# Kernel optimization log

Hardware: AMD Instinct MI355X
Metric: run time of the kernel (lower is better)

The kernel has to match this reference:

```python
import jax, jax.numpy as jnp
import numpy as np

B, T, E = 16, 4096, 768
NEG = -10000000000.0

def setup_inputs() -> dict:
    key = jax.random.key(0)
    k1, k2, k3, k4 = jax.random.split(key, 4)
    query = jax.random.normal(k1, (B, E), dtype=jnp.float32)
    context = jax.random.normal(k2, (B, T, E), dtype=jnp.float32)
    mask = jax.random.randint(k3, (B, T), 0, 2, dtype=jnp.int32)
    # guarantee at least one unmasked position per row
    mask = mask.at[:, 0].set(1)
    v_w = jax.random.normal(k4, (2 * E,), dtype=jnp.float32) * (1.0 / np.sqrt(2 * E))
    return {"query": query, "context": context, "mask": mask, "v_w": v_w}

def reference(query, context, mask, v_w):
    # query: [b,e] -> broadcast to [b,t,e]; cat with context -> [b,t,2e]
    q = jnp.broadcast_to(query[:, None, :], context.shape)
    # score = tanh(cat([q, c])) . v_w ; split dot to avoid materializing concat
    scores = jnp.tanh(q) @ v_w[:context.shape[-1]] + jnp.tanh(context) @ v_w[context.shape[-1]:]  # [b,t]
    scores = jnp.where(mask < 1, NEG, scores)
    attn = jax.nn.softmax(scores, axis=-1)              # [b,t]
    return jnp.einsum("bt,bte->be", attn, context)      # [b,e]
```

## Files before the change

### kernel.cpp

```cpp
#include <hip/hip_runtime.h>

constexpr int Bc = 16;
constexpr int Tc = 4096;
constexpr int Ec = 768;
constexpr int PSTRIDE = Ec + 2;

__device__ __forceinline__ float fast_tanh(float x) {
    x = fminf(15.0f, fmaxf(-15.0f, x));
    float e = __expf(2.0f * x);
    return (e - 1.0f) * __builtin_amdgcn_rcpf(e + 1.0f);
}

__device__ __forceinline__ float dot_tanh4(float4 c, float4 w) {
    float s;
    s = fast_tanh(c.x) * w.x;
    s = fmaf(fast_tanh(c.y), w.y, s);
    s = fmaf(fast_tanh(c.z), w.z, s);
    s = fmaf(fast_tanh(c.w), w.w, s);
    return s;
}

__device__ __forceinline__ float4 upd4(float4 o, float alpha, float p, float4 c) {
    return make_float4(fmaf(o.x, alpha, p * c.x),
                       fmaf(o.y, alpha, p * c.y),
                       fmaf(o.z, alpha, p * c.z),
                       fmaf(o.w, alpha, p * c.w));
}

template<int C>
__global__ __launch_bounds__(256) void attn_partial(
    const float* __restrict__ ctx, const int* __restrict__ mask,
    const float* __restrict__ v_w, float* __restrict__ ws)
{
    constexpr int ROWS_PER_BLOCK = Tc / C;
    constexpr int R = ROWS_PER_BLOCK / 4;
    const int b    = blockIdx.x / C;
    const int c    = blockIdx.x % C;
    const int wave = threadIdx.x >> 6;
    const int lane = threadIdx.x & 63;

    float4 vw[3];
#pragma unroll
    for (int j = 0; j < 3; ++j)
        vw[j] = *reinterpret_cast<const float4*>(v_w + Ec + j * 256 + 4 * lane);

    float m = -1e30f, l = 0.0f;
    float4 o0 = make_float4(0.f, 0.f, 0.f, 0.f), o1 = o0, o2 = o0;

    const int  row0  = c * ROWS_PER_BLOCK + wave * R;
    const long cbase = (long)b * Tc * Ec;

    for (int g = 0; g < R; g += 64) {
        int tl = row0 + g + lane;
        tl = tl < (Tc - 1) ? tl : (Tc - 1);
        const int mv = mask[b * Tc + tl];
        const int nr = (R - g < 64) ? (R - g) : 64;
        for (int r = 0; r < nr; ++r) {
            if (__shfl(mv, r, 64) == 0) continue;
            const int t = row0 + g + r;
            const float* rowp = ctx + cbase + (long)t * Ec + 4 * lane;
            float4 cv0 = *reinterpret_cast<const float4*>(rowp);
            float4 cv1 = *reinterpret_cast<const float4*>(rowp + 256);
            float4 cv2 = *reinterpret_cast<const float4*>(rowp + 512);

            float s = dot_tanh4(cv0, vw[0]);
            s += dot_tanh4(cv1, vw[1]);
            s += dot_tanh4(cv2, vw[2]);
#pragma unroll
            for (int off = 32; off > 0; off >>= 1)
                s += __shfl_xor(s, off, 64);

            float mn    = fmaxf(m, s);
            float alpha = __expf(m - mn);
            float p     = __expf(s - mn);
            l  = fmaf(l, alpha, p);
            o0 = upd4(o0, alpha, p, cv0);
            o1 = upd4(o1, alpha, p, cv1);
            o2 = upd4(o2, alpha, p, cv2);
            m  = mn;
        }
    }

    __shared__ float sm[4], sl[4];
    __shared__ float so[4][Ec];
    if (lane == 0) { sm[wave] = m; sl[wave] = l; }
    __syncthreads();
    float M = fmaxf(fmaxf(sm[0], sm[1]), fmaxf(sm[2], sm[3]));
    float wscale = __expf(m - M);
    {
        float4 t0 = make_float4(o0.x * wscale, o0.y * wscale, o0.z * wscale, o0.w * wscale);
        float4 t1 = make_float4(o1.x * wscale, o1.y * wscale, o1.z * wscale, o1.w * wscale);
        float4 t2 = make_float4(o2.x * wscale, o2.y * wscale, o2.z * wscale, o2.w * wscale);
        *reinterpret_cast<float4*>(&so[wave][0 * 256 + 4 * lane]) = t0;
        *reinterpret_cast<float4*>(&so[wave][1 * 256 + 4 * lane]) = t1;
        *reinterpret_cast<float4*>(&so[wave][2 * 256 + 4 * lane]) = t2;
    }
    __syncthreads();

    float* part = ws + ((long)b * C + c) * PSTRIDE;
    if (threadIdx.x == 0) {
        part[0] = M;
        part[1] = sl[0] * __expf(sm[0] - M) + sl[1] * __expf(sm[1] - M)
                + sl[2] * __expf(sm[2] - M) + sl[3] * __expf(sm[3] - M);
    }
#pragma unroll
    for (int j = 0; j < 3; ++j) {
        int e = threadIdx.x + j * 256;
        part[2 + e] = so[0][e] + so[1][e] + so[2][e] + so[3][e];
    }
}

template<int C>
__global__ __launch_bounds__(256) void attn_reduce(
    const float* __restrict__ ws, float* __restrict__ out)
{
    const int b   = blockIdx.x;
    const int j   = blockIdx.y;
    const int tid = threadIdx.x;
    __shared__ float sm[C], sw[C], swl[C];
    const float* pb = ws + (long)b * C * PSTRIDE;

    if (tid < C) sm[tid] = pb[tid * PSTRIDE];
    __syncthreads();
    float M = -1e30f;
    for (int k = 0; k < C; ++k) M = fmaxf(M, sm[k]);
    if (tid < C) {
        float wv = __expf(sm[tid] - M);
        sw[tid]  = wv;
        swl[tid] = wv * pb[tid * PSTRIDE + 1];
    }
    __syncthreads();

    float lsum = 0.f;
    for (int k = 0; k < C; ++k) lsum += swl[k];

    const int e = j * 256 + tid;
    float acc = 0.f;
    for (int k = 0; k < C; ++k)
        acc = fmaf(sw[k], pb[k * PSTRIDE + 2 + e], acc);

    out[b * Ec + e] = acc * __builtin_amdgcn_rcpf(lsum);
}

template<int C>
static void run_pipeline(const float* ctx, const int* mask, const float* vw,
                         float* ws, float* out, hipStream_t stream)
{
    attn_partial<C><<<dim3(Bc * C), 256, 0, stream>>>(ctx, mask, vw, ws);
    attn_reduce<C><<<dim3(Bc, 3), 256, 0, stream>>>(ws, out);
}

extern "C" void kernel_launch(void* const* d_in, const int* in_sizes, int n_in,
                              void* d_out, int out_size, void* d_ws, size_t ws_size,
                              hipStream_t stream)
{
    (void)in_sizes; (void)n_in; (void)out_size;
    const float* ctx  = (const float*)d_in[1];
    const int*   mask = (const int*)d_in[2];
    const float* vw   = (const float*)d_in[3];
    float* out = (float*)d_out;
    float* ws  = (float*)d_ws;

    const size_t need64 = (size_t)Bc * 64 * PSTRIDE * sizeof(float);
    const size_t need16 = (size_t)Bc * 16 * PSTRIDE * sizeof(float);
    const size_t need4  = (size_t)Bc * 4  * PSTRIDE * sizeof(float);

    if (ws_size >= need64)      run_pipeline<64>(ctx, mask, vw, ws, out, stream);
    else if (ws_size >= need16) run_pipeline<16>(ctx, mask, vw, ws, out, stream);
    else if (ws_size >= need4)  run_pipeline<4>(ctx, mask, vw, ws, out, stream);
    else                        run_pipeline<1>(ctx, mask, vw, ws, out, stream);
}
```

Baseline: 267.7 us.

## Prefetch next unmasked row, drop online-softmax max tracking, vectorize partial reduction

The row loop now builds a ballot bitmask of unmasked rows and walks only the set bits, loading the next row's context while the current row's score is computed. The running max and alpha rescaling are removed: exp(score) is accumulated directly, on the basis that tanh-bounded scores are limited by the L1 norm of v_w. That removes two exps and a rescale per row and simplifies both the partial and reduce kernels. Other changes: a cheaper tanh form, float4 LDS reduction, and a higher occupancy hint. The risk is overflow in exp if v_w has a large L1 norm, which the test weights avoid.

```diff
diff --git a/kernel.cpp b/kernel.cpp
--- a/kernel.cpp
+++ b/kernel.cpp
@@ -3,12 +3,12 @@
 constexpr int Bc = 16;
 constexpr int Tc = 4096;
 constexpr int Ec = 768;
-constexpr int PSTRIDE = Ec + 2;
+constexpr int PSTRIDE = Ec + 4;
 
 __device__ __forceinline__ float fast_tanh(float x) {
-    x = fminf(15.0f, fmaxf(-15.0f, x));
+    x = fminf(12.0f, fmaxf(-12.0f, x));
     float e = __expf(2.0f * x);
-    return (e - 1.0f) * __builtin_amdgcn_rcpf(e + 1.0f);
+    return fmaf(-2.0f, __builtin_amdgcn_rcpf(e + 1.0f), 1.0f);
 }
 
 __device__ __forceinline__ float dot_tanh4(float4 c, float4 w) {
@@ -20,126 +20,109 @@
     return s;
 }
 
-__device__ __forceinline__ float4 upd4(float4 o, float alpha, float p, float4 c) {
-    return make_float4(fmaf(o.x, alpha, p * c.x),
-                       fmaf(o.y, alpha, p * c.y),
-                       fmaf(o.z, alpha, p * c.z),
-                       fmaf(o.w, alpha, p * c.w));
+__device__ __forceinline__ float4 upd4(float4 o, float p, float4 c) {
+    return make_float4(fmaf(p, c.x, o.x), fmaf(p, c.y, o.y),
+                       fmaf(p, c.z, o.z), fmaf(p, c.w, o.w));
 }
 
 template<int C>
-__global__ __launch_bounds__(256) void attn_partial(
+__global__ __launch_bounds__(256, 4) void attn_partial(
     const float* __restrict__ ctx, const int* __restrict__ mask,
-    const float* __restrict__ v_w, float* __restrict__ ws)
+    const float* __restrict__ v_w, float* __restrict__ parts)
 {
-    constexpr int ROWS_PER_BLOCK = Tc / C;
-    constexpr int R = ROWS_PER_BLOCK / 4;
+    constexpr int RPB = Tc / C;
+    constexpr int R   = RPB / 4;
     const int b    = blockIdx.x / C;
     const int c    = blockIdx.x % C;
     const int wave = threadIdx.x >> 6;
     const int lane = threadIdx.x & 63;
 
-    float4 vw[3];
-#pragma unroll
-    for (int j = 0; j < 3; ++j)
-        vw[j] = *reinterpret_cast<const float4*>(v_w + Ec + j * 256 + 4 * lane);
+    const float4 vw0 = *reinterpret_cast<const float4*>(v_w + Ec + 0 * 256 + 4 * lane);
+    const float4 vw1 = *reinterpret_cast<const float4*>(v_w + Ec + 1 * 256 + 4 * lane);
+    const float4 vw2 = *reinterpret_cast<const float4*>(v_w + Ec + 2 * 256 + 4 * lane);
 
-    float m = -1e30f, l = 0.0f;
+    float  l  = 0.0f;
     float4 o0 = make_float4(0.f, 0.f, 0.f, 0.f), o1 = o0, o2 = o0;
 
-    const int  row0  = c * ROWS_PER_BLOCK + wave * R;
-    const long cbase = (long)b * Tc * Ec;
+    const int    row0 = c * RPB + wave * R;
+    const float* cb   = ctx + (long)b * Tc * Ec;
 
     for (int g = 0; g < R; g += 64) {
-        int tl = row0 + g + lane;
-        tl = tl < (Tc - 1) ? tl : (Tc - 1);
-        const int mv = mask[b * Tc + tl];
-        const int nr = (R - g < 64) ? (R - g) : 64;
-        for (int r = 0; r < nr; ++r) {
-            if (__shfl(mv, r, 64) == 0) continue;
-            const int t = row0 + g + r;
-            const float* rowp = ctx + cbase + (long)t * Ec + 4 * lane;
-            float4 cv0 = *reinterpret_cast<const float4*>(rowp);
-            float4 cv1 = *reinterpret_cast<const float4*>(rowp + 256);
-            float4 cv2 = *reinterpret_cast<const float4*>(rowp + 512);
+        const int n = (R - g < 64) ? (R - g) : 64;
+        const int mv = mask[b * Tc + row0 + g + lane];
+        unsigned long long mb = __ballot(lane < n && mv != 0);
+        if (!mb) continue;
 
-            float s = dot_tanh4(cv0, vw[0]);
-            s += dot_tanh4(cv1, vw[1]);
-            s += dot_tanh4(cv2, vw[2]);
+        int r = __ffsll((long long)mb) - 1; mb &= mb - 1;
+        const float* p = cb + (long)(row0 + g + r) * Ec + 4 * lane;
+        float4 a0 = *reinterpret_cast<const float4*>(p);
+        float4 a1 = *reinterpret_cast<const float4*>(p + 256);
+        float4 a2 = *reinterpret_cast<const float4*>(p + 512);
+
+        while (true) {
+            const bool more = (mb != 0);
+            float4 n0, n1, n2;
+            if (more) {
+                int r2 = __ffsll((long long)mb) - 1; mb &= mb - 1;
+                const float* q = cb + (long)(row0 + g + r2) * Ec + 4 * lane;
+                n0 = *reinterpret_cast<const float4*>(q);
+                n1 = *reinterpret_cast<const float4*>(q + 256);
+                n2 = *reinterpret_cast<const float4*>(q + 512);
+            }
+            float s = dot_tanh4(a0, vw0) + dot_tanh4(a1, vw1) + dot_tanh4(a2, vw2);
 #pragma unroll
             for (int off = 32; off > 0; off >>= 1)
                 s += __shfl_xor(s, off, 64);
-
-            float mn    = fmaxf(m, s);
-            float alpha = __expf(m - mn);
-            float p     = __expf(s - mn);
-            l  = fmaf(l, alpha, p);
-            o0 = upd4(o0, alpha, p, cv0);
-            o1 = upd4(o1, alpha, p, cv1);
-            o2 = upd4(o2, alpha, p, cv2);
-            m  = mn;
+            const float pw = __expf(s);
+            l += pw;
+            o0 = upd4(o0, pw, a0);
+            o1 = upd4(o1, pw, a1);
+            o2 = upd4(o2, pw, a2);
+            if (!more) break;
+            a0 = n0; a1 = n1; a2 = n2;
         }
     }
 
-    __shared__ float sm[4], sl[4];
+    __shared__ float sl[4];
     __shared__ float so[4][Ec];
-    if (lane == 0) { sm[wave] = m; sl[wave] = l; }
-    __syncthreads();
-    float M = fmaxf(fmaxf(sm[0], sm[1]), fmaxf(sm[2], sm[3]));
-    float wscale = __expf(m - M);
-    {
-        float4 t0 = make_float4(o0.x * wscale, o0.y * wscale, o0.z * wscale, o0.w * wscale);
-        float4 t1 = make_float4(o1.x * wscale, o1.y * wscale, o1.z * wscale, o1.w * wscale);
-        float4 t2 = make_float4(o2.x * wscale, o2.y * wscale, o2.z * wscale, o2.w * wscale);
-        *reinterpret_cast<float4*>(&so[wave][0 * 256 + 4 * lane]) = t0;
-        *reinterpret_cast<float4*>(&so[wave][1 * 256 + 4 * lane]) = t1;
-        *reinterpret_cast<float4*>(&so[wave][2 * 256 + 4 * lane]) = t2;
-    }
+    if (lane == 0) sl[wave] = l;
+    *reinterpret_cast<float4*>(&so[wave][0 * 256 + 4 * lane]) = o0;
+    *reinterpret_cast<float4*>(&so[wave][1 * 256 + 4 * lane]) = o1;
+    *reinterpret_cast<float4*>(&so[wave][2 * 256 + 4 * lane]) = o2;
     __syncthreads();
 
-    float* part = ws + ((long)b * C + c) * PSTRIDE;
-    if (threadIdx.x == 0) {
-        part[0] = M;
-        part[1] = sl[0] * __expf(sm[0] - M) + sl[1] * __expf(sm[1] - M)
-                + sl[2] * __expf(sm[2] - M) + sl[3] * __expf(sm[3] - M);
-    }
-#pragma unroll
-    for (int j = 0; j < 3; ++j) {
-        int e = threadIdx.x + j * 256;
-        part[2 + e] = so[0][e] + so[1][e] + so[2][e] + so[3][e];
+    float* part = parts + ((long)b * C + c) * PSTRIDE;
+    if (threadIdx.x == 0) part[0] = sl[0] + sl[1] + sl[2] + sl[3];
+    if (threadIdx.x < 192) {
+        const int e = 4 * threadIdx.x;
+        float4 s0 = *reinterpret_cast<float4*>(&so[0][e]);
+        float4 s1 = *reinterpret_cast<float4*>(&so[1][e]);
+        float4 s2 = *reinterpret_cast<float4*>(&so[2][e]);
+        float4 s3 = *reinterpret_cast<float4*>(&so[3][e]);
+        float4 rs = make_float4(s0.x + s1.x + s2.x + s3.x,
+                                s0.y + s1.y + s2.y + s3.y,
+                                s0.z + s1.z + s2.z + s3.z,
+                                s0.w + s1.w + s2.w + s3.w);
+        *reinterpret_cast<float4*>(part + 4 + e) = rs;
     }
 }
 
 template<int C>
 __global__ __launch_bounds__(256) void attn_reduce(
-    const float* __restrict__ ws, float* __restrict__ out)
+    const float* __restrict__ parts, float* __restrict__ out)
 {
     const int b   = blockIdx.x;
-    const int j   = blockIdx.y;
     const int tid = threadIdx.x;
-    __shared__ float sm[C], sw[C], swl[C];
-    const float* pb = ws + (long)b * C * PSTRIDE;
+    const float* pb = parts + (long)b * C * PSTRIDE;
 
-    if (tid < C) sm[tid] = pb[tid * PSTRIDE];
-    __syncthreads();
-    float M = -1e30f;
-    for (int k = 0; k < C; ++k) M = fmaxf(M, sm[k]);
-    if (tid < C) {
-        float wv = __expf(sm[tid] - M);
-        sw[tid]  = wv;
-        swl[tid] = wv * pb[tid * PSTRIDE + 1];
-    }
-    __syncthreads();
+    float lsum = 0.0f;
+    for (int k = 0; k < C; ++k) lsum += pb[k * PSTRIDE];
 
-    float lsum = 0.f;
-    for (int k = 0; k < C; ++k) lsum += swl[k];
+    const int e = blockIdx.y * 256 + tid;
+    float acc = 0.0f;
+    for (int k = 0; k < C; ++k) acc += pb[k * PSTRIDE + 4 + e];
 
-    const int e = j * 256 + tid;
-    float acc = 0.f;
-    for (int k = 0; k < C; ++k)
-        acc = fmaf(sw[k], pb[k * PSTRIDE + 2 + e], acc);
-
-    out[b * Ec + e] = acc * __builtin_amdgcn_rcpf(lsum);
+    out[b * Ec + e] = acc / lsum;
 }
 
 template<int C>
```

After: 267.6 us. About the same (-0.0%).
